# Optimization experiments

Hardware: AMD Instinct MI355X
Metric: run time of the kernel (lower is better)

The kernel has to match this reference:

```python
import jax, jax.numpy as jnp
import numpy as np

N_NODES = 100000
N_EDGES = 1600000
D = 64


def _gcn_norm(edge_index, edge_weight, num_nodes):
    # PyG GCNConv default: add self-loops (weight 1), symmetric deg^-1/2 norm.
    src, dst = edge_index[0], edge_index[1]
    loop = jnp.arange(num_nodes, dtype=edge_index.dtype)
    src = jnp.concatenate([src, loop])
    dst = jnp.concatenate([dst, loop])
    w = jnp.concatenate([edge_weight, jnp.ones((num_nodes,), edge_weight.dtype)])
    deg = jax.ops.segment_sum(w, dst, num_segments=num_nodes)
    dinv = jnp.where(deg > 0, jax.lax.rsqrt(deg), 0.0)
    norm = dinv[src] * w * dinv[dst]  # [E + N]
    return src, dst, norm


def _gcn_conv(h, src, dst, norm, W, b, num_nodes):
    h = h @ W                                   # [N, C_out] linear transform first
    msg = h[src] * norm[:, None]                # gather + scale  [E+N, C_out]
    out = jax.ops.segment_sum(msg, dst, num_segments=num_nodes)  # scatter-add
    return out + b


def setup_inputs() -> dict:
    key = jax.random.key(0)
    ks = jax.random.split(key, 9)
    x = jax.random.normal(ks[0], (N_NODES, D), dtype=jnp.float32)
    edge_index = jax.random.randint(ks[1], (2, N_EDGES), 0, N_NODES, dtype=jnp.int32)
    edge_weight = jax.random.uniform(ks[2], (N_EDGES,), dtype=jnp.float32)
    s = 1.0 / np.sqrt(D)
    W1 = jax.random.uniform(ks[3], (D, D), jnp.float32, -s, s)
    b1 = jnp.zeros((D,), jnp.float32)
    W2 = jax.random.uniform(ks[4], (D, D), jnp.float32, -s, s)
    b2 = jnp.zeros((D,), jnp.float32)
    W3 = jax.random.uniform(ks[5], (D, 1), jnp.float32, -s, s)
    b3 = jnp.zeros((1,), jnp.float32)
    return {"x": x, "edge_index": edge_index, "edge_weight": edge_weight,
            "W1": W1, "b1": b1, "W2": W2, "b2": b2, "W3": W3, "b3": b3}


def reference(x, edge_index, edge_weight, W1, b1, W2, b2, W3, b3):
    n = x.shape[0]
    src, dst, norm = _gcn_norm(edge_index, edge_weight, n)
    h = _gcn_conv(x, src, dst, norm, W1, b1, n)
    h = jax.nn.relu(h)
    h = _gcn_conv(h, src, dst, norm, W2, b2, n)
    h = jax.nn.relu(h)
    h = _gcn_conv(h, src, dst, norm, W3, b3, n)
    return jax.nn.sigmoid(h)  # [N, 1]
```

## Files before the change

### kernel.cpp

```cpp
#include <hip/hip_runtime.h>
#include <hip/hip_fp16.h>
#include <math.h>

#define NN 100000
#define NE 1600000
#define D 64
#define BSH 8
#define NBIN 391
#define EB 8192
#define NBB ((NE + EB - 1) / EB)

typedef _Float16 f16x8 __attribute__((ext_vector_type(8)));
typedef float f32x4 __attribute__((ext_vector_type(4)));
typedef int   i32x4 __attribute__((ext_vector_type(4)));
typedef float fl32x4 __attribute__((ext_vector_type(4)));

__device__ __forceinline__ int2 ldnt2(const int2* p) {
    unsigned long long r = __builtin_nontemporal_load((const unsigned long long*)p);
    int2 o;
    o.x = (int)(unsigned)(r & 0xffffffffu);
    o.y = (int)(unsigned)(r >> 32);
    return o;
}

__global__ void k_binhist(const int* __restrict__ dst, int* __restrict__ counts, int E) {
    __shared__ int h[NBIN];
    for (int i = threadIdx.x; i < NBIN; i += blockDim.x) h[i] = 0;
    __syncthreads();
    int e0 = blockIdx.x * EB;
    int e1 = min(e0 + EB, E);
    for (int e = e0 + (int)threadIdx.x * 4; e < e1; e += blockDim.x * 4) {
        i32x4 d4 = __builtin_nontemporal_load((const i32x4*)(dst + e));
        atomicAdd(&h[d4.x >> BSH], 1);
        atomicAdd(&h[d4.y >> BSH], 1);
        atomicAdd(&h[d4.z >> BSH], 1);
        atomicAdd(&h[d4.w >> BSH], 1);
    }
    __syncthreads();
    for (int i = threadIdx.x; i < NBIN; i += blockDim.x)
        counts[blockIdx.x * NBIN + i] = h[i];
}

__global__ void k_binscan(int* __restrict__ counts, int* __restrict__ binStart) {
    __shared__ int tot[512];
    int b = threadIdx.x;
    int sum = 0;
    if (b < NBIN) {
#pragma unroll 8
        for (int k = 0; k < NBB; k++) {
            int idx = k * NBIN + b;
            int c = counts[idx];
            counts[idx] = sum;
            sum += c;
        }
    }
    tot[b] = (b < NBIN) ? sum : 0;
    __syncthreads();
    int v = tot[b];
    for (int off = 1; off < 512; off <<= 1) {
        int add = (b >= off) ? tot[b - off] : 0;
        __syncthreads();
        tot[b] += add;
        __syncthreads();
    }
    if (b < NBIN) binStart[b] = tot[b] - v;
    if (b == NBIN - 1) binStart[NBIN] = tot[b];
}

__global__ void k_binscatter(const int* __restrict__ src, const int* __restrict__ dst,
                             const float* __restrict__ w, const int* __restrict__ counts,
                             const int* __restrict__ binStart, int2* __restrict__ binned,
                             int E) {
    __shared__ int cur[NBIN];
    for (int i = threadIdx.x; i < NBIN; i += blockDim.x)
        cur[i] = binStart[i] + counts[blockIdx.x * NBIN + i];
    __syncthreads();
    int e0 = blockIdx.x * EB;
    int e1 = min(e0 + EB, E);
    for (int e = e0 + (int)threadIdx.x * 4; e < e1; e += blockDim.x * 4) {
        i32x4  d4 = __builtin_nontemporal_load((const i32x4*)(dst + e));
        i32x4  s4 = __builtin_nontemporal_load((const i32x4*)(src + e));
        fl32x4 w4 = __builtin_nontemporal_load((const fl32x4*)(w + e));
        int pos;
        pos = atomicAdd(&cur[d4.x >> BSH], 1);
        binned[pos] = make_int2(((d4.x & 255) << 17) | s4.x, __float_as_int(w4.x));
        pos = atomicAdd(&cur[d4.y >> BSH], 1);
        binned[pos] = make_int2(((d4.y & 255) << 17) | s4.y, __float_as_int(w4.y));
        pos = atomicAdd(&cur[d4.z >> BSH], 1);
        binned[pos] = make_int2(((d4.z & 255) << 17) | s4.z, __float_as_int(w4.z));
        pos = atomicAdd(&cur[d4.w >> BSH], 1);
        binned[pos] = make_int2(((d4.w & 255) << 17) | s4.w, __float_as_int(w4.w));
    }
}

__global__ void k_degcsr(const int2* __restrict__ binned, const int* __restrict__ binStart,
                         float* __restrict__ dinv, int* __restrict__ row_ptr,
                         int2* __restrict__ edges, int n) {
    __shared__ int   cnt[256];
    __shared__ float ws[256];
    __shared__ int   off[256];
    __shared__ int   rp[256];
    int b = blockIdx.x, t = threadIdx.x;
    cnt[t] = 0; ws[t] = 0.0f;
    __syncthreads();
    int e0 = binStart[b], e1 = binStart[b + 1];
    for (int e = e0 + t; e < e1; e += 256) {
        int2 r = binned[e];
        int dlow = (unsigned)r.x >> 17;
        atomicAdd(&cnt[dlow], 1);
        atomicAdd(&ws[dlow], __int_as_float(r.y));
    }
    __syncthreads();
    int v = cnt[t];
    off[t] = v;
    __syncthreads();
    for (int o = 1; o < 256; o <<= 1) {
        int add = (t >= o) ? off[t - o] : 0;
        __syncthreads();
        off[t] += add;
        __syncthreads();
    }
    int node = b * 256 + t;
    rp[t] = e0 + off[t] - v;
    if (node < n) {
        dinv[node] = rsqrtf(1.0f + ws[t]);
        row_ptr[node] = rp[t];
    }
    if (b == NBIN - 1 && t == 0) row_ptr[n] = binStart[NBIN];
    cnt[t] = 0;
    __syncthreads();
    for (int e = e0 + t; e < e1; e += 256) {
        int2 r = binned[e];
        int dlow = (unsigned)r.x >> 17;
        int rank = atomicAdd(&cnt[dlow], 1);
        edges[rp[dlow] + rank] = make_int2(r.x & 0x1FFFF, r.y);
    }
}

template <int IN_HALF>
__global__ void k_gemm(const void* __restrict__ Xv, const float* __restrict__ W,
                       const float* __restrict__ dinv, __half* __restrict__ T, int n) {
    int wid = (int)((blockIdx.x * blockDim.x + threadIdx.x) >> 6);
    int lane = threadIdx.x & 63;
    int col16 = lane & 15, kg = lane >> 4;
    int r0 = wid * 32;
    if (r0 >= n) return;
    f16x8 bf[2][4];
#pragma unroll
    for (int kk = 0; kk < 2; kk++)
#pragma unroll
        for (int ct = 0; ct < 4; ct++) {
            f16x8 b;
#pragma unroll
            for (int j = 0; j < 8; j++)
                b[j] = (_Float16)W[(size_t)(kk * 32 + kg * 8 + j) * D + ct * 16 + col16];
            bf[kk][ct] = b;
        }
#pragma unroll
    for (int tt = 0; tt < 2; tt++) {
        int row = r0 + tt * 16 + col16;
        f16x8 a0, a1;
        if (IN_HALF) {
            const _Float16* xr = (const _Float16*)Xv + (size_t)row * D;
            a0 = *(const f16x8*)(xr + kg * 8);
            a1 = *(const f16x8*)(xr + 32 + kg * 8);
        } else {
            const float* xr = (const float*)Xv + (size_t)row * D;
#pragma unroll
            for (int j = 0; j < 8; j++) {
                a0[j] = (_Float16)xr[kg * 8 + j];
                a1[j] = (_Float16)xr[32 + kg * 8 + j];
            }
        }
        float dvr[4];
#pragma unroll
        for (int r = 0; r < 4; r++) dvr[r] = dinv[r0 + tt * 16 + kg * 4 + r];
#pragma unroll
        for (int ct = 0; ct < 4; ct++) {
            f32x4 z = {0.0f, 0.0f, 0.0f, 0.0f};
            z = __builtin_amdgcn_mfma_f32_16x16x32_f16(a0, bf[0][ct], z, 0, 0, 0);
            z = __builtin_amdgcn_mfma_f32_16x16x32_f16(a1, bf[1][ct], z, 0, 0, 0);
            __half* to = T + (size_t)(r0 + tt * 16 + kg * 4) * D + ct * 16 + col16;
#pragma unroll
            for (int r = 0; r < 4; r++)
                to[(size_t)r * D] = __float2half(z[r] * dvr[r]);
        }
    }
}

template <int FUSE_W3>
__global__ void k_agg(const __half2* __restrict__ T2, const int* __restrict__ row_ptr,
                      const int2* __restrict__ edges, const float* __restrict__ dinv,
                      const float* __restrict__ bias, const float* __restrict__ W3,
                      void* __restrict__ outv, int n) {
    int wave = (int)((blockIdx.x * blockDim.x + threadIdx.x) >> 6);
    int lane = threadIdx.x & 63;
    if (wave >= n) return;
    int c = lane & 31;
    int h = lane >> 5;
    int beg = row_ptr[wave], end = row_ptr[wave + 1];
    float ax = 0.0f, ay = 0.0f, bx = 0.0f, by = 0.0f;
    int i = beg;
    for (; i + 16 <= end; i += 16) {
        int2 er[8];
#pragma unroll
        for (int j = 0; j < 8; j++) er[j] = ldnt2(&edges[i + 2 * j + h]);
        __half2 tv[8];
#pragma unroll
        for (int j = 0; j < 8; j++) tv[j] = T2[(size_t)er[j].x * 32 + c];
#pragma unroll
        for (int j = 0; j < 8; j++) {
            float nv = __int_as_float(er[j].y);
            float2 f = __half22float2(tv[j]);
            if (j & 1) { bx += nv * f.x; by += nv * f.y; }
            else       { ax += nv * f.x; ay += nv * f.y; }
        }
    }
    if (i + 8 <= end) {
        int2 er[4];
#pragma unroll
        for (int j = 0; j < 4; j++) er[j] = ldnt2(&edges[i + 2 * j + h]);
        __half2 tv[4];
#pragma unroll
        for (int j = 0; j < 4; j++) tv[j] = T2[(size_t)er[j].x * 32 + c];
#pragma unroll
        for (int j = 0; j < 4; j++) {
            float nv = __int_as_float(er[j].y);
            float2 f = __half22float2(tv[j]);
            if (j & 1) { bx += nv * f.x; by += nv * f.y; }
            else       { ax += nv * f.x; ay += nv * f.y; }
        }
        i += 8;
    }
    if (i + 4 <= end) {
        int2 er[2];
#pragma unroll
        for (int j = 0; j < 2; j++) er[j] = ldnt2(&edges[i + 2 * j + h]);
#pragma unroll
        for (int j = 0; j < 2; j++) {
            float nv = __int_as_float(er[j].y);
            float2 f = __half22float2(T2[(size_t)er[j].x * 32 + c]);
            if (j & 1) { bx += nv * f.x; by += nv * f.y; }
            else       { ax += nv * f.x; ay += nv * f.y; }
        }
        i += 4;
    }
    if (i + 2 <= end) {
        int2 e = ldnt2(&edges[i + h]);
        float nv = __int_as_float(e.y);
        float2 f = __half22float2(T2[(size_t)e.x * 32 + c]);
        ax += nv * f.x; ay += nv * f.y;
        i += 2;
    }
    if (i < end && h == 0) {
        int2 e = ldnt2(&edges[i]);
        float nv = __int_as_float(e.y);
        float2 f = __half22float2(T2[(size_t)e.x * 32 + c]);
        ax += nv * f.x; ay += nv * f.y;
    }
    ax += bx; ay += by;
    ax += __shfl_xor(ax, 32);
    ay += __shfl_xor(ay, 32);
    float dv = dinv[wave];
    float2 self = __half22float2(T2[(size_t)wave * 32 + c]);
    float hx = fmaxf(dv * (ax + self.x) + bias[2 * c], 0.0f);
    float hy = fmaxf(dv * (ay + self.y) + bias[2 * c + 1], 0.0f);
    if (FUSE_W3) {
        float pp = hx * W3[2 * c] + hy * W3[2 * c + 1];
#pragma unroll
        for (int off = 16; off; off >>= 1) pp += __shfl_xor(pp, off);
        if (lane == 0) ((float*)outv)[wave] = dv * pp;
    } else {
        if (lane < 32) ((__half2*)outv)[(size_t)wave * 32 + c] = __floats2half2_rn(hx, hy);
    }
}

__global__ void k_agg3(const float* __restrict__ t3, const int* __restrict__ row_ptr,
                       const int2* __restrict__ edges, const float* __restrict__ dinv,
                       const float* __restrict__ b3, float* __restrict__ out, int n) {
    int v = blockIdx.x * blockDim.x + threadIdx.x;
    if (v >= n) return;
    float acc0 = t3[v];
    float acc1 = 0.0f;
    int beg = row_ptr[v], end = row_ptr[v + 1];
    int i = beg;
    for (; i + 8 <= end; i += 8) {
        int2 er[8]; float av[8];
#pragma unroll
        for (int j = 0; j < 8; j++) er[j] = ldnt2(&edges[i + j]);
#pragma unroll
        for (int j = 0; j < 8; j++) av[j] = t3[er[j].x];
#pragma unroll
        for (int j = 0; j < 8; j++) {
            if (j & 1) acc1 += __int_as_float(er[j].y) * av[j];
            else       acc0 += __int_as_float(er[j].y) * av[j];
        }
    }
    for (; i < end; i++) {
        int2 e = ldnt2(&edges[i]);
        acc0 += __int_as_float(e.y) * t3[e.x];
    }
    float z = dinv[v] * (acc0 + acc1) + b3[0];
    out[v] = 1.0f / (1.0f + expf(-z));
}

extern "C" void kernel_launch(void* const* d_in, const int* in_sizes, int n_in,
                              void* d_out, int out_size, void* d_ws, size_t ws_size,
                              hipStream_t stream) {
    const float* x  = (const float*)d_in[0];
    const int*   ei = (const int*)d_in[1];
    const float* w  = (const float*)d_in[2];
    const float* W1 = (const float*)d_in[3];
    const float* b1 = (const float*)d_in[4];
    const float* W2 = (const float*)d_in[5];
    const float* b2 = (const float*)d_in[6];
    const float* W3 = (const float*)d_in[7];
    const float* b3 = (const float*)d_in[8];
    float* out = (float*)d_out;

    const int N = NN, E = NE;
    const int* src = ei;
    const int* dst = ei + E;

    char* p = (char*)d_ws;
    auto alloc = [&](size_t bytes) -> char* {
        char* r = p;
        p += (bytes + 255) & ~(size_t)255;
        return r;
    };
    float* dinv    = (float*)alloc((size_t)N * 4);
    int*   row_ptr = (int*)alloc((size_t)(N + 1) * 4);
    int*   binStart= (int*)alloc((NBIN + 1) * 4);
    int*   counts  = (int*)alloc((size_t)NBB * NBIN * 4);
    int2*  binned  = (int2*)alloc((size_t)E * 8);
    int2*  edges   = (int2*)alloc((size_t)E * 8);
    __half* bufA   = (__half*)alloc((size_t)N * D * 2);
    __half* bufB   = (__half*)alloc((size_t)N * D * 2);
    float* t3      = (float*)alloc((size_t)N * 4);

    const int BT = 256;
    int gN = (N + BT - 1) / BT;
    int gW = (N * 64 + BT - 1) / BT;
    int nWaves = (N + 31) / 32;
    int gG = (nWaves * 64 + BT - 1) / BT;

    k_binhist<<<NBB, BT, 0, stream>>>(dst, counts, E);
    k_binscan<<<1, 512, 0, stream>>>(counts, binStart);
    k_binscatter<<<NBB, BT, 0, stream>>>(src, dst, w, counts, binStart, binned, E);
    k_degcsr<<<NBIN, BT, 0, stream>>>(binned, binStart, dinv, row_ptr, edges, N);

    k_gemm<0><<<gG, BT, 0, stream>>>(x, W1, dinv, bufA, N);
    k_agg<0><<<gW, BT, 0, stream>>>((const __half2*)bufA, row_ptr, edges, dinv, b1, nullptr, bufB, N);
    k_gemm<1><<<gG, BT, 0, stream>>>(bufB, W2, dinv, bufA, N);
    k_agg<1><<<gW, BT, 0, stream>>>((const __half2*)bufA, row_ptr, edges, dinv, b2, W3, t3, N);
    k_agg3<<<gN, BT, 0, stream>>>(t3, row_ptr, edges, dinv, b3, out, N);
}
```

Measured before the change: 212.3 us.

## Parallelize bin-count scan across bins and halve edge block size

Replaces the single-block serial scan over per-block bin counts with one block per bin that scans its column in parallel, followed by a small second scan over bin totals. The counts matrix is transposed to bin-major so each bin's counts are contiguous. Edge block size is halved to 4096, which doubles the histogram and scatter grid, gives more parallelism there, and adds one extra kernel launch. The new scan assumes NBB is at most 512, and with EB=4096 NBB is 391, so this holds.

```diff
diff --git a/kernel.cpp b/kernel.cpp
--- a/kernel.cpp
+++ b/kernel.cpp
@@ -7,7 +7,7 @@
 #define D 64
 #define BSH 8
 #define NBIN 391
-#define EB 8192
+#define EB 4096
 #define NBB ((NE + EB - 1) / EB)
 
 typedef _Float16 f16x8 __attribute__((ext_vector_type(8)));
@@ -38,33 +38,42 @@
     }
     __syncthreads();
     for (int i = threadIdx.x; i < NBIN; i += blockDim.x)
-        counts[blockIdx.x * NBIN + i] = h[i];
-}
-
-__global__ void k_binscan(int* __restrict__ counts, int* __restrict__ binStart) {
-    __shared__ int tot[512];
-    int b = threadIdx.x;
-    int sum = 0;
-    if (b < NBIN) {
-#pragma unroll 8
-        for (int k = 0; k < NBB; k++) {
-            int idx = k * NBIN + b;
-            int c = counts[idx];
-            counts[idx] = sum;
-            sum += c;
-        }
-    }
-    tot[b] = (b < NBIN) ? sum : 0;
-    __syncthreads();
-    int v = tot[b];
+        counts[(size_t)i * NBB + blockIdx.x] = h[i];
+}
+
+__global__ void k_binscan(int* __restrict__ counts, int* __restrict__ binTot) {
+    __shared__ int sm[512];
+    int b = blockIdx.x, t = threadIdx.x;
+    int v0 = (t < NBB)       ? counts[(size_t)b * NBB + t] : 0;
+    int v1 = (t + 256 < NBB) ? counts[(size_t)b * NBB + t + 256] : 0;
+    sm[t] = v0; sm[t + 256] = v1;
+    __syncthreads();
     for (int off = 1; off < 512; off <<= 1) {
-        int add = (b >= off) ? tot[b - off] : 0;
-        __syncthreads();
-        tot[b] += add;
-        __syncthreads();
-    }
-    if (b < NBIN) binStart[b] = tot[b] - v;
-    if (b == NBIN - 1) binStart[NBIN] = tot[b];
+        int a0 = (t >= off) ? sm[t - off] : 0;
+        int a1 = (t + 256 >= off) ? sm[t + 256 - off] : 0;
+        __syncthreads();
+        sm[t] += a0; sm[t + 256] += a1;
+        __syncthreads();
+    }
+    if (t < NBB)       counts[(size_t)b * NBB + t] = sm[t] - v0;
+    if (t + 256 < NBB) counts[(size_t)b * NBB + t + 256] = sm[t + 256] - v1;
+    if (t == 0) binTot[b] = sm[511];
+}
+
+__global__ void k_binscan2(const int* __restrict__ binTot, int* __restrict__ binStart) {
+    __shared__ int sm[512];
+    int t = threadIdx.x;
+    int v = (t < NBIN) ? binTot[t] : 0;
+    sm[t] = v;
+    __syncthreads();
+    for (int off = 1; off < 512; off <<= 1) {
+        int add = (t >= off) ? sm[t - off] : 0;
+        __syncthreads();
+        sm[t] += add;
+        __syncthreads();
+    }
+    if (t < NBIN) binStart[t] = sm[t] - v;
+    if (t == NBIN - 1) binStart[NBIN] = sm[t];
 }
 
 __global__ void k_binscatter(const int* __restrict__ src, const int* __restrict__ dst,
@@ -73,7 +82,7 @@
                              int E) {
     __shared__ int cur[NBIN];
     for (int i = threadIdx.x; i < NBIN; i += blockDim.x)
-        cur[i] = binStart[i] + counts[blockIdx.x * NBIN + i];
+        cur[i] = binStart[i] + counts[(size_t)i * NBB + blockIdx.x];
     __syncthreads();
     int e0 = blockIdx.x * EB;
     int e1 = min(e0 + EB, E);
@@ -331,6 +340,7 @@
     float* dinv    = (float*)alloc((size_t)N * 4);
     int*   row_ptr = (int*)alloc((size_t)(N + 1) * 4);
     int*   binStart= (int*)alloc((NBIN + 1) * 4);
+    int*   binTot  = (int*)alloc(NBIN * 4);
     int*   counts  = (int*)alloc((size_t)NBB * NBIN * 4);
     int2*  binned  = (int2*)alloc((size_t)E * 8);
     int2*  edges   = (int2*)alloc((size_t)E * 8);
@@ -345,7 +355,8 @@
     int gG = (nWaves * 64 + BT - 1) / BT;
 
     k_binhist<<<NBB, BT, 0, stream>>>(dst, counts, E);
-    k_binscan<<<1, 512, 0, stream>>>(counts, binStart);
+    k_binscan<<<NBIN, BT, 0, stream>>>(counts, binTot);
+    k_binscan2<<<1, 512, 0, stream>>>(binTot, binStart);
     k_binscatter<<<NBB, BT, 0, stream>>>(src, dst, w, counts, binStart, binned, E);
     k_degcsr<<<NBIN, BT, 0, stream>>>(binned, binStart, dinv, row_ptr, edges, N);
 
```

New measurement: 201.2 us. 5.2% less time.
